# Kernel optimization log

Hardware: AMD Instinct MI355X
Metric: run time of the kernel (lower is better)

Reference implementation:

```python
import jax, jax.numpy as jnp
import numpy as np

SCALE = (4, 4)
PORTION = 0.5


def setup_inputs() -> dict:
    key = jax.random.key(0)
    x = jax.random.normal(key, (16, 512, 64, 64), dtype=jnp.float32)
    return {"x": x}


def _shift_scale(x, s0, s1):
    # x: (b, shift, h, w); cyclic shuffle of the S=s0*s1 channel groups,
    # with a spatially-varying shift amount over the (s0, s1) sub-grid.
    b, c, h, w = x.shape
    S = s0 * s1
    cps = c // S
    # (b, S, cps, s0, h/s0, s1, w/s1)
    y = x.reshape(b, S, cps, s0, h // s0, s1, w // s1)
    # -> (b, S, cps, h/s0, w/s1, s0, s1) -> (b, S, cps, h/s0, w/s1, S)
    y = y.transpose(0, 1, 2, 4, 6, 3, 5).reshape(b, S, cps, h // s0, w // s1, S)
    # index[s, k] = (s + k) mod S  (cyclic gather along last axis)
    idx = (jnp.arange(S)[:, None] + jnp.arange(S)[None, :]) % S
    y = jnp.take_along_axis(y, idx.reshape(1, S, 1, 1, 1, S), axis=5)
    # undo the spatial regrouping: (b, c, h/s0, w/s1, s0, s1) -> (b, c, h, w)
    y = y.reshape(b, c, h // s0, w // s1, s0, s1)
    y = y.transpose(0, 1, 4, 2, 5, 3).reshape(b, c, h, w)
    return y


def reference(x):
    s0, s1 = SCALE
    S = s0 * s1
    b, c, h, w = x.shape
    shift = int(PORTION * c)
    shift = (shift // S) * S  # floor to multiple of S (matches torch code)
    keep_x = x[:, : c - shift]
    shift_x = _shift_scale(x[:, c - shift :], s0, s1)
    return jnp.concatenate([keep_x, shift_x], axis=1)
```

## Files before the change

### kernel.cpp

```cpp
#include <hip/hip_runtime.h>


#define B 16
#define C 512
#define H 64
#define W 64
#define W4 (W / 4)

__global__ __launch_bounds__(256) void GlobalShift2dV2Portion_kernel(
    const float4* __restrict__ in, float4* __restrict__ out) {
    int i = blockIdx.x * 256 + threadIdx.x;
    int w4 = i & 15;
    int t  = i >> 4;
    int h  = t & 63;
    int bc = t >> 6;
    int ch = bc & 511;
    if (ch < 256) {
        out[i] = in[i];
    } else {
        int s     = (ch - 256) >> 4;
        int t_in  = (s + ((h >> 4) << 2) + (w4 >> 2)) & 15;
        int h_in  = ((t_in >> 2) << 4) | (h & 15);
        int w4_in = ((t_in & 3) << 2) | (w4 & 3);
        int j     = ((bc << 6) + h_in) * W4 + w4_in;
        out[i] = in[j];
    }
}

extern "C" void kernel_launch(void* const* d_in, const int* in_sizes, int n_in,
                              void* d_out, int out_size, void* d_ws, size_t ws_size,
                              hipStream_t stream) {
    const float4* in = (const float4*)d_in[0];
    float4* out = (float4*)d_out;
    int total4 = in_sizes[0] / 4;
    int blocks = total4 / 256;
    GlobalShift2dV2Portion_kernel<<<blocks, 256, 0, stream>>>(in, out);
}
```

Baseline: 223.1 us.

## Stage shifted channel planes through LDS with one block per plane

Each block now handles a whole 64x64 channel plane and issues four float4 loads per thread. Planes in the shifted half are first loaded coalesced into shared memory, then permuted on read from LDS, so the scattered global gather is removed. Copied planes stay a straight global copy. The cost is 16 KB of LDS per block, a barrier, and fewer blocks overall, which may reduce occupancy.

```diff
diff --git a/kernel.cpp b/kernel.cpp
--- a/kernel.cpp
+++ b/kernel.cpp
@@ -1,29 +1,40 @@
 #include <hip/hip_runtime.h>
 
 
-#define B 16
-#define C 512
-#define H 64
-#define W 64
-#define W4 (W / 4)
-
 __global__ __launch_bounds__(256) void GlobalShift2dV2Portion_kernel(
     const float4* __restrict__ in, float4* __restrict__ out) {
-    int i = blockIdx.x * 256 + threadIdx.x;
-    int w4 = i & 15;
-    int t  = i >> 4;
-    int h  = t & 63;
-    int bc = t >> 6;
+    __shared__ float4 lds[1024];
+
+    int bc = blockIdx.x;
     int ch = bc & 511;
+    const float4* src = in  + ((size_t)bc << 10);
+    float4*       dst = out + ((size_t)bc << 10);
+    int t = threadIdx.x;
+
     if (ch < 256) {
-        out[i] = in[i];
+        #pragma unroll
+        for (int k = 0; k < 4; ++k) {
+            int o = t + (k << 8);
+            dst[o] = src[o];
+        }
     } else {
-        int s     = (ch - 256) >> 4;
-        int t_in  = (s + ((h >> 4) << 2) + (w4 >> 2)) & 15;
-        int h_in  = ((t_in >> 2) << 4) | (h & 15);
-        int w4_in = ((t_in & 3) << 2) | (w4 & 3);
-        int j     = ((bc << 6) + h_in) * W4 + w4_in;
-        out[i] = in[j];
+        #pragma unroll
+        for (int k = 0; k < 4; ++k) {
+            int o = t + (k << 8);
+            lds[o] = src[o];
+        }
+        __syncthreads();
+        int s = (ch - 256) >> 4;
+        #pragma unroll
+        for (int k = 0; k < 4; ++k) {
+            int o  = t + (k << 8);
+            int w4 = o & 15;
+            int h  = o >> 4;
+            int t_in  = (s + ((h >> 4) << 2) + (w4 >> 2)) & 15;
+            int h_in  = ((t_in >> 2) << 4) | (h & 15);
+            int w4_in = ((t_in & 3) << 2) | (w4 & 3);
+            dst[o] = lds[(h_in << 4) | w4_in];
+        }
     }
 }
 
@@ -32,7 +43,6 @@
                               hipStream_t stream) {
     const float4* in = (const float4*)d_in[0];
     float4* out = (float4*)d_out;
-    int total4 = in_sizes[0] / 4;
-    int blocks = total4 / 256;
+    int blocks = in_sizes[0] / (64 * 64);
     GlobalShift2dV2Portion_kernel<<<blocks, 256, 0, stream>>>(in, out);
 }
```

Measured after the change: 226.8 us. No clear change (+1.7%).
